# Performance work log

Hardware: AMD Instinct MI355X
Metric: run time of the kernel (lower is better)

## Reference

```python
import jax, jax.numpy as jnp
import numpy as np

ALPHA = 0.05
GDEP = 2


def conv1x1(x, w, b):
    # x: [N,C,V,L], w: [O,C], b: [O]
    return jnp.einsum('ncvl,oc->novl', x, w) + b[None, :, None, None]


def setup_inputs() -> dict:
    key = jax.random.key(0)
    ks = jax.random.split(key, 9)
    N, C, V, L = 32, 32, 400, 12
    c_out = 32
    cat = (GDEP + 1) * C
    s = 0.05
    return {
        'x': jax.random.normal(ks[0], (N, C, V, L), jnp.float32),
        'w_lin1': jax.random.normal(ks[1], (C, C), jnp.float32) * s,
        'b_lin1': jnp.zeros((C,), jnp.float32),
        'w_lin2': jax.random.normal(ks[2], (C, C), jnp.float32) * s,
        'b_lin2': jnp.zeros((C,), jnp.float32),
        'w_mlp1': jax.random.normal(ks[3], (c_out, cat), jnp.float32) * s,
        'b_mlp1': jnp.zeros((c_out,), jnp.float32),
        'w_mlp2': jax.random.normal(ks[4], (c_out, cat), jnp.float32) * s,
        'b_mlp2': jnp.zeros((c_out,), jnp.float32),
    }


def reference(x, w_lin1, b_lin1, w_lin2, b_lin2, w_mlp1, b_mlp1, w_mlp2, b_mlp2):
    # dynamic adjacency: adj[n,v,w,l] = sum_c x1[n,c,v,l] * x2[n,c,w,l]
    x1 = jnp.tanh(conv1x1(x, w_lin1, b_lin1))
    x2 = jnp.tanh(conv1x1(x, w_lin2, b_lin2))
    adj = jnp.einsum('ncvl,ncwl->nvwl', x1, x2)  # [N,V,V,L]
    adj0 = jax.nn.softmax(adj, axis=2)
    adj1 = jax.nn.softmax(jnp.swapaxes(adj, 1, 2), axis=2)

    def diffuse(a):
        h = x
        out = [h]
        for _ in range(GDEP):
            # nconv: h[n,c,w,l] = sum_v h[n,c,v,l] * a[n,v,w,l]
            h = ALPHA * x + (1.0 - ALPHA) * jnp.einsum('ncvl,nvwl->ncwl', h, a)
            out.append(h)
        return jnp.concatenate(out, axis=1)  # [N,(GDEP+1)*C,V,L]

    ho1 = conv1x1(diffuse(adj0), w_mlp1, b_mlp1)
    ho2 = conv1x1(diffuse(adj1), w_mlp2, b_mlp2)
    return ho1 + ho2
```

## Files before the change

kernel.cpp:

```cpp
#include <hip/hip_runtime.h>
#include <stdint.h>

#define TT 1024
#define AL 0.05f
#define OM 0.95f
#define STRD 408
#define LOG2E 1.4426950408889634f

typedef short s4v __attribute__((ext_vector_type(4)));
typedef short s8v __attribute__((ext_vector_type(8)));
typedef float f4v __attribute__((ext_vector_type(4)));
typedef float f16v __attribute__((ext_vector_type(16)));
typedef int   i2v __attribute__((ext_vector_type(2)));

#define MF32(a,b,c) __builtin_amdgcn_mfma_f32_32x32x16_bf16(a,b,c,0,0,0)
#define MF16(a,b,c) __builtin_amdgcn_mfma_f32_16x16x32_bf16(a,b,c,0,0,0)

#if __has_builtin(__builtin_amdgcn_exp2f)
#define E2(x) __builtin_amdgcn_exp2f(x)
#else
#define E2(x) exp2f(x)
#endif

__device__ __forceinline__ uint16_t f2bf(float f){ union{float f;uint32_t i;}t; t.f=f; return (uint16_t)((t.i + 0x7fffu + ((t.i>>16)&1u))>>16); }
__device__ __forceinline__ float bf2f(uint16_t h){ union{uint32_t i;float f;}t; t.i=((uint32_t)h)<<16; return t.f; }
__device__ __forceinline__ float bfLO(uint32_t u){ union{uint32_t i;float f;}t; t.i=u<<16; return t.f; }
__device__ __forceinline__ float bfHI(uint32_t u){ union{uint32_t i;float f;}t; t.i=u&0xffff0000u; return t.f; }
__device__ __forceinline__ uint32_t cvtpk(float lo, float hi){ uint32_t r; asm("v_cvt_pk_bf16_f32 %0, %1, %2" : "=v"(r) : "v"(lo), "v"(hi)); return r; }
__device__ __forceinline__ void pl32swap(uint32_t &x, uint32_t &y){
#if __has_builtin(__builtin_amdgcn_permlane32_swap)
  i2v rr = __builtin_amdgcn_permlane32_swap((int)x, (int)y, false, false);
  x = (uint32_t)rr.x; y = (uint32_t)rr.y;
#else
  asm("v_permlane32_swap_b32 %0, %1" : "+v"(x), "+v"(y));
#endif
}
__device__ __forceinline__ float ftanh(float x){ float t = E2(2.885390081777927f*x); return __builtin_fmaf(-2.f, __builtin_amdgcn_rcpf(1.f + t), 1.f); }
__device__ __forceinline__ s8v ld8(const uint16_t* p){ return *(const s8v*)p; }
#define ROWF(e2) (((e2)&3) + 8*((e2)>>2) + 4*h2)
#define VXA(row,off) ((((row)<<5) + (off)) ^ (((row)&7)<<3))

__device__ __align__(16) float gStage[32*12*12800];

#define X1S 0
#define X2S 12800
#define XCV 25600
#define PBA 38656
#define HCV 54656
#define GCV 67712
#define RINV 80768
#define CINV 81168

__global__ __launch_bounds__(TT) void dymix(
    const float* __restrict__ x,
    const float* __restrict__ w1, const float* __restrict__ b1,
    const float* __restrict__ w2, const float* __restrict__ b2,
    const float* __restrict__ wm1, const float* __restrict__ bm1,
    const float* __restrict__ wm2, const float* __restrict__ bm2)
{
  __shared__ __align__(16) uint16_t S[81568];

  const int blk = blockIdx.x;
  const int xcd = blk & 7, slot = blk >> 3;
  const int n = xcd*4 + slot/12;
  const int l = slot - (slot/12)*12;
  const int t = threadIdx.x;
  const int wv = t >> 6;
  const int lane = t & 63;
  const int q  = lane >> 4;
  const int r  = lane & 15;
  const int h2 = lane >> 5;
  const int m32 = lane & 31;
  const long xbase = (long)n*153600 + l;

  for (int i = t; i < 12800; i += TT) {
    int c = i / 400, v = i - c*400;
    S[XCV + c*STRD + v] = f2bf(x[xbase + (long)i*12]);
  }
  __syncthreads();

  for (int i = t; i < 12800; i += TT) { int v = i>>5, c = i&31; S[PBA + VXA(v,c)] = S[XCV + c*STRD + v]; }
  for (int i = t; i < 1024; i += TT) {
    int o = i>>5, c = i&31;
    S[PBA + 12800 + o*40 + c] = f2bf(w1[i]);
    S[PBA + 14080 + o*40 + c] = f2bf(w2[i]);
  }
  if (t < 32) { ((float*)(S+PBA+15360))[t] = b1[t]; ((float*)(S+PBA+15424))[t] = b2[t]; }
  __syncthreads();

  #pragma unroll
  for (int j = 0; j < 2; ++j) {
    int u = wv + 16*j;
    if (u < 24) {
      int nt = u >> 1, li = u & 1;
      const uint16_t* W = S + PBA + 12800 + li*1280;
      const float* bfp = (const float*)(S + PBA + 15360 + li*64);
      uint16_t* dst = S + (li ? X2S : X1S);
      const float osc = li ? 1.f : LOG2E;
      f16v z = {};
      #pragma unroll
      for (int kk = 0; kk < 2; ++kk) {
        s8v a = ld8(W + m32*40 + kk*16 + h2*8);
        s8v b = ld8(S + PBA + VXA(nt*32 + m32, kk*16 + h2*8));
        z = MF32(a, b, z);
      }
      int v = nt*32 + m32;
      #pragma unroll
      for (int g = 0; g < 4; ++g) {
        float p0 = ftanh(z[4*g+0] + bfp[8*g+4*h2+0]) * osc;
        float p1 = ftanh(z[4*g+1] + bfp[8*g+4*h2+1]) * osc;
        float p2 = ftanh(z[4*g+2] + bfp[8*g+4*h2+2]) * osc;
        float p3 = ftanh(z[4*g+3] + bfp[8*g+4*h2+3]) * osc;
        uint2 d; d.x = cvtpk(p0,p1); d.y = cvtpk(p2,p3);
        *(uint2*)(dst + VXA(v, 8*g + 4*h2)) = d;
      }
    } else if (u < 28) {
      int li = (u-24)>>1, mt = u&1;
      const uint16_t* W = S + PBA + 12800 + li*1280;
      const float* bfp = (const float*)(S + PBA + 15360 + li*64);
      uint16_t* dst = S + (li ? X2S : X1S);
      const float osc = li ? 1.f : LOG2E;
      s8v a = ld8(W + (mt*16 + r)*40 + q*8);
      s8v b = ld8(S + PBA + VXA(384 + r, q*8));
      f4v z4 = {}; z4 = MF16(a, b, z4);
      float p0 = ftanh(z4[0] + bfp[mt*16+q*4+0]) * osc;
      float p1 = ftanh(z4[1] + bfp[mt*16+q*4+1]) * osc;
      float p2 = ftanh(z4[2] + bfp[mt*16+q*4+2]) * osc;
      float p3 = ftanh(z4[3] + bfp[mt*16+q*4+3]) * osc;
      uint2 d; d.x = cvtpk(p0,p1); d.y = cvtpk(p2,p3);
      *(uint2*)(dst + VXA(384 + r, mt*16 + q*4)) = d;
    }
  }
  s8v xf0, xf1, xft;
  {
    int m0 = (wv < 12) ? wv : 0;
    xf0 = ld8(S + PBA + VXA(m0*32 + m32, h2*8));
    xf1 = ld8(S + PBA + VXA(m0*32 + m32, 16 + h2*8));
    xft = ld8(S + PBA + VXA(384 + r, q*8));
  }
  __syncthreads();

  float* rsf = (float*)(S + HCV);
  float* csf = rsf + 400;
  for (int i = t; i < 400; i += TT) csf[i] = 0.f;
  __syncthreads();
  {
    s8v av[2]; f4v rac[2] = {{},{}};
    #pragma unroll
    for (int jj = 0; jj < 2; ++jj) { int vt = wv + 16*jj; if (vt < 25) av[jj] = ld8(S + X1S + VXA(vt*16 + r, q*8)); }
    for (int wt = 0; wt < 25; ++wt) {
      s8v b = ld8(S + X2S + VXA(wt*16 + r, q*8));
      float cp = 0.f;
      #pragma unroll
      for (int jj = 0; jj < 2; ++jj) {
        int vt = wv + 16*jj;
        if (vt < 25) {
          f4v z = {}; z = MF16(av[jj], b, z);
          #pragma unroll
          for (int e = 0; e < 4; ++e) { float ev = E2(z[e]); rac[jj][e] += ev; cp += ev; }
        }
      }
      cp += __shfl_xor(cp, 16); cp += __shfl_xor(cp, 32);
      if (q == 0) atomicAdd(&csf[wt*16 + r], cp);
    }
    #pragma unroll
    for (int jj = 0; jj < 2; ++jj) {
      int vt = wv + 16*jj;
      if (vt < 25) {
        #pragma unroll
        for (int e = 0; e < 4; ++e) {
          float s = rac[jj][e];
          s += __shfl_xor(s,1); s += __shfl_xor(s,2); s += __shfl_xor(s,4); s += __shfl_xor(s,8);
          if (r == 0) rsf[vt*16 + q*4 + e] = s;
        }
      }
    }
  }
  __syncthreads();
  for (int i = t; i < 400; i += TT) { S[RINV + i] = f2bf(1.f/rsf[i]); S[CINV + i] = f2bf(1.f/csf[i]); }
  __syncthreads();

  f16v acc[2];
  for (int step = 0; step < 2; ++step) {
    { f16v zv = {}; acc[0]=zv; acc[1]=zv; }
    const uint16_t* AH = S + (step ? HCV : XCV);
    const uint16_t* AG = S + (step ? GCV : XCV);
    for (int sb = 0; sb < 13; ++sb) {
      const int vbase = sb*32;
      const bool lastsb = (sb == 12);
      const int kmax = lastsb ? 1 : 2;
      s8v fr[2][2];
      uint2 td0[2], td1[2];
      #pragma unroll
      for (int jj = 0; jj < 2; ++jj) {
        int g = wv + 16*jj;
        if (g >= 26) continue;
        int chain = (g < 13) ? 0 : 1;
        int uu = g - 13*chain;
        const uint16_t* sa = S + (chain ? X2S : X1S);
        const uint16_t* sb2 = S + (chain ? X1S : X2S);
        const int scl = chain ? CINV : RINV;
        if (uu < 12) {
          s8v a0 = ld8(sa + VXA(vbase + m32, h2*8));
          s8v a1 = ld8(sa + VXA(vbase + m32, 16 + h2*8));
          s8v b0 = ld8(sb2 + VXA(uu*32 + m32, h2*8));
          s8v b1 = ld8(sb2 + VXA(uu*32 + m32, 16 + h2*8));
          f16v z = {}; z = MF32(a0, b0, z); z = MF32(a1, b1, z);
          #pragma unroll
          for (int k = 0; k < 2; ++k) {
            if (k < kmax) {
              const uint16_t* spt = S + scl + vbase + 16*k + 4*h2;
              uint32_t sAB = *(const uint32_t*)(spt);
              uint32_t sCD = *(const uint32_t*)(spt + 2);
              uint32_t sEF = *(const uint32_t*)(spt + 8);
              uint32_t sGH = *(const uint32_t*)(spt + 10);
              uint32_t C0 = cvtpk(E2(z[8*k+0])*bfLO(sAB), E2(z[8*k+1])*bfHI(sAB));
              uint32_t C1 = cvtpk(E2(z[8*k+2])*bfLO(sCD), E2(z[8*k+3])*bfHI(sCD));
              uint32_t C2 = cvtpk(E2(z[8*k+4])*bfLO(sEF), E2(z[8*k+5])*bfHI(sEF));
              uint32_t C3 = cvtpk(E2(z[8*k+6])*bfLO(sGH), E2(z[8*k+7])*bfHI(sGH));
              pl32swap(C0, C2);
              pl32swap(C1, C3);
              union { uint32_t d[4]; s8v v8; } F;
              F.d[0] = C0; F.d[1] = C1; F.d[2] = C2; F.d[3] = C3;
              fr[jj][k] = F.v8;
            }
          }
        } else {
          s8v bT = ld8(sb2 + VXA(384 + r, q*8));
          td1[jj].x = 0u; td1[jj].y = 0u;
          {
            s8v a = ld8(sa + VXA(vbase + r, q*8));
            f4v z4 = {}; z4 = MF16(a, bT, z4);
            float p0 = E2(z4[0]) * bf2f(S[scl + vbase + q*4 + 0]);
            float p1 = E2(z4[1]) * bf2f(S[scl + vbase + q*4 + 1]);
            float p2 = E2(z4[2]) * bf2f(S[scl + vbase + q*4 + 2]);
            float p3 = E2(z4[3]) * bf2f(S[scl + vbase + q*4 + 3]);
            td0[jj].x = cvtpk(p0,p1); td0[jj].y = cvtpk(p2,p3);
          }
          if (!lastsb) {
            s8v a = ld8(sa + VXA(vbase + 16 + r, q*8));
            f4v z4 = {}; z4 = MF16(a, bT, z4);
            float p0 = E2(z4[0]) * bf2f(S[scl + vbase + 16 + q*4 + 0]);
            float p1 = E2(z4[1]) * bf2f(S[scl + vbase + 16 + q*4 + 1]);
            float p2 = E2(z4[2]) * bf2f(S[scl + vbase + 16 + q*4 + 2]);
            float p3 = E2(z4[3]) * bf2f(S[scl + vbase + 16 + q*4 + 3]);
            td1[jj].x = cvtpk(p0,p1); td1[jj].y = cvtpk(p2,p3);
          }
        }
      }
      #pragma unroll
      for (int jj = 0; jj < 2; ++jj) {
        int g = wv + 16*jj;
        if (g >= 26) continue;
        int chain = (g < 13) ? 0 : 1;
        int uu = g - 13*chain;
        const uint16_t* Acv = chain ? AG : AH;
        if (uu < 12) {
          #pragma unroll
          for (int k = 0; k < 2; ++k) {
            if (k < kmax) {
              s8v a = ld8(Acv + m32*STRD + vbase + k*16 + h2*8);
              acc[jj] = MF32(a, fr[jj][k], acc[jj]);
            }
          }
        } else {
          const int src0 = (((q<<1)) & 3)*16 + r;
          const int src1 = (((q<<1)+1) & 3)*16 + r;
          uint32_t a0x = (uint32_t)__shfl((int)td0[jj].x, src0);
          uint32_t a0y = (uint32_t)__shfl((int)td0[jj].y, src0);
          uint32_t a1x = (uint32_t)__shfl((int)td1[jj].x, src0);
          uint32_t a1y = (uint32_t)__shfl((int)td1[jj].y, src0);
          uint32_t b0x = (uint32_t)__shfl((int)td0[jj].x, src1);
          uint32_t b0y = (uint32_t)__shfl((int)td0[jj].y, src1);
          uint32_t b1x = (uint32_t)__shfl((int)td1[jj].x, src1);
          uint32_t b1y = (uint32_t)__shfl((int)td1[jj].y, src1);
          const bool hi = (q >= 2);
          union { uint32_t u[4]; s8v v8; } B;
          B.u[0] = hi ? a1x : a0x;
          B.u[1] = hi ? a1y : a0y;
          B.u[2] = hi ? b1x : b0x;
          B.u[3] = hi ? b1y : b0y;
          #pragma unroll
          for (int mt2 = 0; mt2 < 2; ++mt2) {
            int koff = (lastsb && q >= 2) ? 0 : q*8;
            s8v a = ld8(Acv + (mt2*16 + r)*STRD + vbase + koff);
            f4v c4 = { acc[jj][4*mt2+0], acc[jj][4*mt2+1], acc[jj][4*mt2+2], acc[jj][4*mt2+3] };
            c4 = MF16(a, B.v8, c4);
            acc[jj][4*mt2+0]=c4[0]; acc[jj][4*mt2+1]=c4[1]; acc[jj][4*mt2+2]=c4[2]; acc[jj][4*mt2+3]=c4[3];
          }
        }
      }
    }
    __syncthreads();
    if (step == 0) {
      #pragma unroll
      for (int jj = 0; jj < 2; ++jj) {
        int g = wv + 16*jj;
        if (g >= 26) continue;
        int chain = (g < 13) ? 0 : 1;
        int uu = g - 13*chain;
        uint16_t* dst = S + (chain ? GCV : HCV);
        if (uu < 12) {
          int w = uu*32 + m32;
          #pragma unroll
          for (int e2 = 0; e2 < 16; ++e2) {
            int c = ROWF(e2);
            dst[c*STRD + w] = f2bf(AL*bf2f(S[XCV + c*STRD + w]) + OM*acc[jj][e2]);
          }
        } else {
          int w = 384 + r;
          #pragma unroll
          for (int mt2 = 0; mt2 < 2; ++mt2)
            #pragma unroll
            for (int e = 0; e < 4; ++e) {
              int c = mt2*16 + q*4 + e;
              dst[c*STRD + w] = f2bf(AL*bf2f(S[XCV + c*STRD + w]) + OM*acc[jj][4*mt2+e]);
            }
        }
      }
      __syncthreads();
    }
  }

  for (int i = t; i < 12800; i += TT) {
    int v = i >> 5, c = i & 31;
    int d = VXA(v, c);
    S[X1S + d] = S[HCV + c*STRD + v];
    S[X2S + d] = S[GCV + c*STRD + v];
  }
  #pragma unroll
  for (int jj = 0; jj < 2; ++jj) {
    int g = wv + 16*jj;
    if (g >= 26) continue;
    int chain = (g < 13) ? 0 : 1;
    int uu = g - 13*chain;
    uint16_t* dst = S + (chain ? PBA : XCV);
    if (uu < 12) {
      int w = uu*32 + m32;
      #pragma unroll
      for (int gg = 0; gg < 4; ++gg) {
        uint2 d;
        d.x = cvtpk(OM*acc[jj][4*gg+0], OM*acc[jj][4*gg+1]);
        d.y = cvtpk(OM*acc[jj][4*gg+2], OM*acc[jj][4*gg+3]);
        *(uint2*)(dst + VXA(w, 8*gg + 4*h2)) = d;
      }
    } else {
      int w = 384 + r;
      #pragma unroll
      for (int mt2 = 0; mt2 < 2; ++mt2) {
        uint2 d;
        d.x = cvtpk(OM*acc[jj][4*mt2+0], OM*acc[jj][4*mt2+1]);
        d.y = cvtpk(OM*acc[jj][4*mt2+2], OM*acc[jj][4*mt2+3]);
        *(uint2*)(dst + VXA(w, mt2*16 + q*4)) = d;
      }
    }
  }
  __syncthreads();
  for (int i = t; i < 1024; i += TT) {
    int o = i >> 5, c = i & 31;
    float h2w = wm1[o*96 + 64 + c], g2w = wm2[o*96 + 64 + c];
    S[HCV +        o*40 + c] = f2bf(wm1[o*96 + c] + wm2[o*96 + c] + AL*(h2w + g2w));
    S[HCV + 1280 + o*40 + c] = f2bf(wm1[o*96 + 32 + c]);
    S[HCV + 2560 + o*40 + c] = f2bf(h2w);
    S[HCV + 3840 + o*40 + c] = f2bf(wm2[o*96 + 32 + c]);
    S[HCV + 5120 + o*40 + c] = f2bf(g2w);
  }
  if (t < 32) ((float*)(S + HCV + 6400))[t] = bm1[t] + bm2[t];
  __syncthreads();

  {
    const float* boF = (const float*)(S + HCV + 6400);
    float* oSl = gStage + (long)(n*12 + l)*12800;
    const int fb[5] = { 0, X1S, XCV, X2S, PBA };
    int m = wv;
    if (m < 12) {
      f16v z = {};
      #pragma unroll
      for (int p = 0; p < 5; ++p) {
        #pragma unroll
        for (int kk = 0; kk < 2; ++kk) {
          s8v a = ld8(S + HCV + p*1280 + m32*40 + kk*16 + h2*8);
          s8v b;
          if (p == 0) b = kk ? xf1 : xf0;
          else        b = ld8(S + fb[p] + VXA(m*32 + m32, kk*16 + h2*8));
          z = MF32(a, b, z);
        }
      }
      int v = m*32 + m32;
      #pragma unroll
      for (int e2 = 0; e2 < 16; ++e2) {
        int o = ROWF(e2);
        oSl[o*400 + v] = z[e2] + boF[o];
      }
    } else if (m < 14) {
      int mt = m - 12;
      f4v z4 = {};
      #pragma unroll
      for (int p = 0; p < 5; ++p) {
        s8v a = ld8(S + HCV + p*1280 + (mt*16 + r)*40 + q*8);
        s8v b = (p == 0) ? xft : ld8(S + fb[p] + VXA(384 + r, q*8));
        z4 = MF16(a, b, z4);
      }
      #pragma unroll
      for (int e = 0; e < 4; ++e) {
        int o = mt*16 + q*4 + e;
        oSl[o*400 + 384 + r] = z4[e] + boF[o];
      }
    }
  }
}

__global__ __launch_bounds__(256) void finT(float* __restrict__ out) {
  int idx = blockIdx.x*256 + threadIdx.x;
  int n = idx / 12800, ov = idx - n*12800;
  const float* src = gStage + (long)n*153600 + ov;
  float vals[12];
  #pragma unroll
  for (int l = 0; l < 12; ++l) vals[l] = src[(long)l*12800];
  float4* dst = (float4*)(out + (long)idx*12);
  dst[0] = make_float4(vals[0],vals[1],vals[2],vals[3]);
  dst[1] = make_float4(vals[4],vals[5],vals[6],vals[7]);
  dst[2] = make_float4(vals[8],vals[9],vals[10],vals[11]);
}

extern "C" void kernel_launch(void* const* d_in, const int* in_sizes, int n_in,
                              void* d_out, int out_size, void* d_ws, size_t ws_size,
                              hipStream_t stream) {
  (void)in_sizes; (void)n_in; (void)out_size; (void)d_ws; (void)ws_size;
  dymix<<<dim3(384), dim3(TT), 0, stream>>>(
      (const float*)d_in[0],
      (const float*)d_in[1], (const float*)d_in[2],
      (const float*)d_in[3], (const float*)d_in[4],
      (const float*)d_in[5], (const float*)d_in[6],
      (const float*)d_in[7], (const float*)d_in[8]);
  finT<<<dim3(1600), dim3(256), 0, stream>>>((float*)d_out);
}
```

Baseline: 231.5 us.

## Use FP8 MFMA for adjacency scores and shrink LDS footprint

Stores the tanh projections x1/x2 as FP8 in shared memory and computes the adjacency logits with FP8 MFMA instead of BF16. It also restructures the shared-memory layout to roughly half the size. Weights are now read directly from global memory instead of staged copies. The final MLP is split into two passes that reuse buffers, with the second pass accumulating into the global staging output. The aim is to raise occupancy and cut LDS traffic and MFMA cost, at the risk of reduced accuracy in the softmax logits and an extra global read-modify-write.

```diff
diff --git a/kernel.cpp b/kernel.cpp
--- a/kernel.cpp
+++ b/kernel.cpp
@@ -15,6 +15,8 @@
 
 #define MF32(a,b,c) __builtin_amdgcn_mfma_f32_32x32x16_bf16(a,b,c,0,0,0)
 #define MF16(a,b,c) __builtin_amdgcn_mfma_f32_16x16x32_bf16(a,b,c,0,0,0)
+#define MFP32(a,b,c) __builtin_amdgcn_mfma_f32_32x32x16_fp8_fp8(a,b,c,0,0,0)
+#define MFP16(a,b,c) __builtin_amdgcn_mfma_f32_16x16x32_fp8_fp8(a,b,c,0,0,0)
 
 #if __has_builtin(__builtin_amdgcn_exp2f)
 #define E2(x) __builtin_amdgcn_exp2f(x)
@@ -37,19 +39,50 @@
 }
 __device__ __forceinline__ float ftanh(float x){ float t = E2(2.885390081777927f*x); return __builtin_fmaf(-2.f, __builtin_amdgcn_rcpf(1.f + t), 1.f); }
 __device__ __forceinline__ s8v ld8(const uint16_t* p){ return *(const s8v*)p; }
+
+__device__ __forceinline__ uint32_t sw1fp8(float f){
+  union{float f;uint32_t u;}t; t.f=f;
+  uint32_t sgn=(t.u>>24)&0x80u; uint32_t a=t.u&0x7fffffffu;
+  union{uint32_t u;float f;}af; af.u=a;
+  if(af.f>448.f) return sgn|0x7eu;
+  if(af.f<0.001953125f){ int q=(int)(af.f*512.f+0.5f); if(q>7)q=7; return sgn|(uint32_t)q; }
+  uint32_t lsb=(a>>20)&1u; a+=0x0007ffffu+lsb;
+  int ex=(int)(a>>23)-120; uint32_t man=(a>>20)&7u;
+  if(ex>15||(ex==15&&man==7u)) return sgn|0x7eu;
+  if(ex<=0){ int q=(int)(af.f*512.f+0.5f); if(q>7)q=7; return sgn|(uint32_t)q; }
+  return sgn|((uint32_t)ex<<3)|man;
+}
+__device__ __forceinline__ uint32_t pk4fp8(float a,float b,float c,float d){
+#if __has_builtin(__builtin_amdgcn_cvt_pk_fp8_f32)
+  int v = __builtin_amdgcn_cvt_pk_fp8_f32(a,b,0,false);
+  v = __builtin_amdgcn_cvt_pk_fp8_f32(c,d,v,true);
+  return (uint32_t)v;
+#else
+  return sw1fp8(a) | (sw1fp8(b)<<8) | (sw1fp8(c)<<16) | (sw1fp8(d)<<24);
+#endif
+}
+__device__ __forceinline__ s8v packw8(float4 f0, float4 f1){
+  union{uint32_t d[4]; s8v v8;} A;
+  A.d[0]=cvtpk(f0.x,f0.y); A.d[1]=cvtpk(f0.z,f0.w);
+  A.d[2]=cvtpk(f1.x,f1.y); A.d[3]=cvtpk(f1.z,f1.w);
+  return A.v8;
+}
+
 #define ROWF(e2) (((e2)&3) + 8*((e2)>>2) + 4*h2)
 #define VXA(row,off) ((((row)<<5) + (off)) ^ (((row)&7)<<3))
+#define VX8(row,b) ((((row)<<5) + (b)) ^ (((row)&3)<<4))
 
 __device__ __align__(16) float gStage[32*12*12800];
 
-#define X1S 0
-#define X2S 12800
-#define XCV 25600
-#define PBA 38656
-#define HCV 54656
-#define GCV 67712
-#define RINV 80768
-#define CINV 81168
+#define X1B 0
+#define X2B 12800
+#define XCV 12800
+#define GCV 25856
+#define XTU 25856
+#define RINV 38912
+#define CINV 39312
+#define HV 0
+#define F2V 12800
 
 __global__ __launch_bounds__(TT) void dymix(
     const float* __restrict__ x,
@@ -58,7 +91,8 @@
     const float* __restrict__ wm1, const float* __restrict__ bm1,
     const float* __restrict__ wm2, const float* __restrict__ bm2)
 {
-  __shared__ __align__(16) uint16_t S[81568];
+  __shared__ __align__(16) uint16_t S[39712];
+  uint8_t* S8 = (uint8_t*)S;
 
   const int blk = blockIdx.x;
   const int xcd = blk & 7, slot = blk >> 3;
@@ -79,13 +113,7 @@
   }
   __syncthreads();
 
-  for (int i = t; i < 12800; i += TT) { int v = i>>5, c = i&31; S[PBA + VXA(v,c)] = S[XCV + c*STRD + v]; }
-  for (int i = t; i < 1024; i += TT) {
-    int o = i>>5, c = i&31;
-    S[PBA + 12800 + o*40 + c] = f2bf(w1[i]);
-    S[PBA + 14080 + o*40 + c] = f2bf(w2[i]);
-  }
-  if (t < 32) { ((float*)(S+PBA+15360))[t] = b1[t]; ((float*)(S+PBA+15424))[t] = b2[t]; }
+  for (int i = t; i < 12800; i += TT) { int v = i>>5, c = i&31; S[XTU + VXA(v,c)] = S[XCV + c*STRD + v]; }
   __syncthreads();
 
   #pragma unroll
@@ -93,69 +121,71 @@
     int u = wv + 16*j;
     if (u < 24) {
       int nt = u >> 1, li = u & 1;
-      const uint16_t* W = S + PBA + 12800 + li*1280;
-      const float* bfp = (const float*)(S + PBA + 15360 + li*64);
-      uint16_t* dst = S + (li ? X2S : X1S);
+      const float* wsrc = li ? w2 : w1;
+      const float* bsrc = li ? b2 : b1;
+      uint8_t* dst8 = S8 + (li ? X2B : X1B);
       const float osc = li ? 1.f : LOG2E;
       f16v z = {};
       #pragma unroll
       for (int kk = 0; kk < 2; ++kk) {
-        s8v a = ld8(W + m32*40 + kk*16 + h2*8);
-        s8v b = ld8(S + PBA + VXA(nt*32 + m32, kk*16 + h2*8));
+        const float* wp = wsrc + m32*32 + kk*16 + h2*8;
+        s8v a = packw8(*(const float4*)(wp), *(const float4*)(wp+4));
+        s8v b = ld8(S + XTU + VXA(nt*32 + m32, kk*16 + h2*8));
         z = MF32(a, b, z);
       }
       int v = nt*32 + m32;
       #pragma unroll
       for (int g = 0; g < 4; ++g) {
-        float p0 = ftanh(z[4*g+0] + bfp[8*g+4*h2+0]) * osc;
-        float p1 = ftanh(z[4*g+1] + bfp[8*g+4*h2+1]) * osc;
-        float p2 = ftanh(z[4*g+2] + bfp[8*g+4*h2+2]) * osc;
-        float p3 = ftanh(z[4*g+3] + bfp[8*g+4*h2+3]) * osc;
-        uint2 d; d.x = cvtpk(p0,p1); d.y = cvtpk(p2,p3);
-        *(uint2*)(dst + VXA(v, 8*g + 4*h2)) = d;
+        float4 bv = *(const float4*)(bsrc + 8*g + 4*h2);
+        float p0 = ftanh(z[4*g+0] + bv.x) * osc;
+        float p1 = ftanh(z[4*g+1] + bv.y) * osc;
+        float p2 = ftanh(z[4*g+2] + bv.z) * osc;
+        float p3 = ftanh(z[4*g+3] + bv.w) * osc;
+        *(uint32_t*)(dst8 + VX8(v, 8*g + 4*h2)) = pk4fp8(p0,p1,p2,p3);
       }
     } else if (u < 28) {
       int li = (u-24)>>1, mt = u&1;
-      const uint16_t* W = S + PBA + 12800 + li*1280;
-      const float* bfp = (const float*)(S + PBA + 15360 + li*64);
-      uint16_t* dst = S + (li ? X2S : X1S);
+      const float* wsrc = li ? w2 : w1;
+      const float* bsrc = li ? b2 : b1;
+      uint8_t* dst8 = S8 + (li ? X2B : X1B);
       const float osc = li ? 1.f : LOG2E;
-      s8v a = ld8(W + (mt*16 + r)*40 + q*8);
-      s8v b = ld8(S + PBA + VXA(384 + r, q*8));
+      const float* wp = wsrc + (mt*16 + r)*32 + q*8;
+      s8v a = packw8(*(const float4*)(wp), *(const float4*)(wp+4));
+      s8v b = ld8(S + XTU + VXA(384 + r, q*8));
       f4v z4 = {}; z4 = MF16(a, b, z4);
-      float p0 = ftanh(z4[0] + bfp[mt*16+q*4+0]) * osc;
-      float p1 = ftanh(z4[1] + bfp[mt*16+q*4+1]) * osc;
-      float p2 = ftanh(z4[2] + bfp[mt*16+q*4+2]) * osc;
-      float p3 = ftanh(z4[3] + bfp[mt*16+q*4+3]) * osc;
-      uint2 d; d.x = cvtpk(p0,p1); d.y = cvtpk(p2,p3);
-      *(uint2*)(dst + VXA(384 + r, mt*16 + q*4)) = d;
+      float4 bv = *(const float4*)(bsrc + mt*16 + q*4);
+      float p0 = ftanh(z4[0] + bv.x) * osc;
+      float p1 = ftanh(z4[1] + bv.y) * osc;
+      float p2 = ftanh(z4[2] + bv.z) * osc;
+      float p3 = ftanh(z4[3] + bv.w) * osc;
+      *(uint32_t*)(dst8 + VX8(384 + r, mt*16 + q*4)) = pk4fp8(p0,p1,p2,p3);
     }
   }
   s8v xf0, xf1, xft;
   {
     int m0 = (wv < 12) ? wv : 0;
-    xf0 = ld8(S + PBA + VXA(m0*32 + m32, h2*8));
-    xf1 = ld8(S + PBA + VXA(m0*32 + m32, 16 + h2*8));
-    xft = ld8(S + PBA + VXA(384 + r, q*8));
-  }
-  __syncthreads();
-
-  float* rsf = (float*)(S + HCV);
+    xf0 = ld8(S + XTU + VXA(m0*32 + m32, h2*8));
+    xf1 = ld8(S + XTU + VXA(m0*32 + m32, 16 + h2*8));
+    xft = ld8(S + XTU + VXA(384 + r, q*8));
+  }
+  __syncthreads();
+
+  float* rsf = (float*)(S + GCV);
   float* csf = rsf + 400;
   for (int i = t; i < 400; i += TT) csf[i] = 0.f;
   __syncthreads();
   {
-    s8v av[2]; f4v rac[2] = {{},{}};
+    long av8[2]; f4v rac[2] = {{},{}};
     #pragma unroll
-    for (int jj = 0; jj < 2; ++jj) { int vt = wv + 16*jj; if (vt < 25) av[jj] = ld8(S + X1S + VXA(vt*16 + r, q*8)); }
+    for (int jj = 0; jj < 2; ++jj) { int vt = wv + 16*jj; if (vt < 25) av8[jj] = *(const long*)(S8 + X1B + VX8(vt*16 + r, q*8)); }
     for (int wt = 0; wt < 25; ++wt) {
-      s8v b = ld8(S + X2S + VXA(wt*16 + r, q*8));
+      long b8 = *(const long*)(S8 + X2B + VX8(wt*16 + r, q*8));
       float cp = 0.f;
       #pragma unroll
       for (int jj = 0; jj < 2; ++jj) {
         int vt = wv + 16*jj;
         if (vt < 25) {
-          f4v z = {}; z = MF16(av[jj], b, z);
+          f4v z = {}; z = MFP16(av8[jj], b8, z);
           #pragma unroll
           for (int e = 0; e < 4; ++e) { float ev = E2(z[e]); rac[jj][e] += ev; cp += ev; }
         }
@@ -183,7 +213,7 @@
   f16v acc[2];
   for (int step = 0; step < 2; ++step) {
     { f16v zv = {}; acc[0]=zv; acc[1]=zv; }
-    const uint16_t* AH = S + (step ? HCV : XCV);
+    const uint16_t* AH = S + XCV;
     const uint16_t* AG = S + (step ? GCV : XCV);
     for (int sb = 0; sb < 13; ++sb) {
       const int vbase = sb*32;
@@ -197,15 +227,15 @@
         if (g >= 26) continue;
         int chain = (g < 13) ? 0 : 1;
         int uu = g - 13*chain;
-        const uint16_t* sa = S + (chain ? X2S : X1S);
-        const uint16_t* sb2 = S + (chain ? X1S : X2S);
+        const uint8_t* sa8 = S8 + (chain ? X2B : X1B);
+        const uint8_t* sb8 = S8 + (chain ? X1B : X2B);
         const int scl = chain ? CINV : RINV;
         if (uu < 12) {
-          s8v a0 = ld8(sa + VXA(vbase + m32, h2*8));
-          s8v a1 = ld8(sa + VXA(vbase + m32, 16 + h2*8));
-          s8v b0 = ld8(sb2 + VXA(uu*32 + m32, h2*8));
-          s8v b1 = ld8(sb2 + VXA(uu*32 + m32, 16 + h2*8));
-          f16v z = {}; z = MF32(a0, b0, z); z = MF32(a1, b1, z);
+          long a0 = *(const long*)(sa8 + VX8(vbase + m32, h2*8));
+          long a1 = *(const long*)(sa8 + VX8(vbase + m32, 16 + h2*8));
+          long b0 = *(const long*)(sb8 + VX8(uu*32 + m32, h2*8));
+          long b1 = *(const long*)(sb8 + VX8(uu*32 + m32, 16 + h2*8));
+          f16v z = {}; z = MFP32(a0, b0, z); z = MFP32(a1, b1, z);
           #pragma unroll
           for (int k = 0; k < 2; ++k) {
             if (k < kmax) {
@@ -226,11 +256,11 @@
             }
           }
         } else {
-          s8v bT = ld8(sb2 + VXA(384 + r, q*8));
+          long bT = *(const long*)(sb8 + VX8(384 + r, q*8));
           td1[jj].x = 0u; td1[jj].y = 0u;
           {
-            s8v a = ld8(sa + VXA(vbase + r, q*8));
-            f4v z4 = {}; z4 = MF16(a, bT, z4);
+            long a = *(const long*)(sa8 + VX8(vbase + r, q*8));
+            f4v z4 = {}; z4 = MFP16(a, bT, z4);
             float p0 = E2(z4[0]) * bf2f(S[scl + vbase + q*4 + 0]);
             float p1 = E2(z4[1]) * bf2f(S[scl + vbase + q*4 + 1]);
             float p2 = E2(z4[2]) * bf2f(S[scl + vbase + q*4 + 2]);
@@ -238,8 +268,8 @@
             td0[jj].x = cvtpk(p0,p1); td0[jj].y = cvtpk(p2,p3);
           }
           if (!lastsb) {
-            s8v a = ld8(sa + VXA(vbase + 16 + r, q*8));
-            f4v z4 = {}; z4 = MF16(a, bT, z4);
+            long a = *(const long*)(sa8 + VX8(vbase + 16 + r, q*8));
+            f4v z4 = {}; z4 = MFP16(a, bT, z4);
             float p0 = E2(z4[0]) * bf2f(S[scl + vbase + 16 + q*4 + 0]);
             float p1 = E2(z4[1]) * bf2f(S[scl + vbase + 16 + q*4 + 1]);
             float p2 = E2(z4[2]) * bf2f(S[scl + vbase + 16 + q*4 + 2]);
@@ -299,13 +329,12 @@
         if (g >= 26) continue;
         int chain = (g < 13) ? 0 : 1;
         int uu = g - 13*chain;
-        uint16_t* dst = S + (chain ? GCV : HCV);
         if (uu < 12) {
           int w = uu*32 + m32;
           #pragma unroll
           for (int e2 = 0; e2 < 16; ++e2) {
             int c = ROWF(e2);
-            dst[c*STRD + w] = f2bf(AL*bf2f(S[XCV + c*STRD + w]) + OM*acc[jj][e2]);
+            acc[jj][e2] = AL*bf2f(S[XCV + c*STRD + w]) + OM*acc[jj][e2];
           }
         } else {
           int w = 384 + r;
@@ -314,27 +343,42 @@
             #pragma unroll
             for (int e = 0; e < 4; ++e) {
               int c = mt2*16 + q*4 + e;
-              dst[c*STRD + w] = f2bf(AL*bf2f(S[XCV + c*STRD + w]) + OM*acc[jj][4*mt2+e]);
+              acc[jj][4*mt2+e] = AL*bf2f(S[XCV + c*STRD + w]) + OM*acc[jj][4*mt2+e];
             }
         }
       }
       __syncthreads();
-    }
-  }
-
-  for (int i = t; i < 12800; i += TT) {
-    int v = i >> 5, c = i & 31;
-    int d = VXA(v, c);
-    S[X1S + d] = S[HCV + c*STRD + v];
-    S[X2S + d] = S[GCV + c*STRD + v];
-  }
+      #pragma unroll
+      for (int jj = 0; jj < 2; ++jj) {
+        int g = wv + 16*jj;
+        if (g >= 26) continue;
+        int chain = (g < 13) ? 0 : 1;
+        int uu = g - 13*chain;
+        uint16_t* dst = S + (chain ? GCV : XCV);
+        if (uu < 12) {
+          int w = uu*32 + m32;
+          #pragma unroll
+          for (int e2 = 0; e2 < 16; ++e2) { int c = ROWF(e2); dst[c*STRD + w] = f2bf(acc[jj][e2]); }
+        } else {
+          int w = 384 + r;
+          #pragma unroll
+          for (int mt2 = 0; mt2 < 2; ++mt2)
+            #pragma unroll
+            for (int e = 0; e < 4; ++e) { int c = mt2*16 + q*4 + e; dst[c*STRD + w] = f2bf(acc[jj][4*mt2+e]); }
+        }
+      }
+      __syncthreads();
+    }
+  }
+
+  for (int i = t; i < 12800; i += TT) { int v = i >> 5, c = i & 31; S[HV + VXA(v,c)] = S[XCV + c*STRD + v]; }
+  __syncthreads();
   #pragma unroll
   for (int jj = 0; jj < 2; ++jj) {
     int g = wv + 16*jj;
-    if (g >= 26) continue;
-    int chain = (g < 13) ? 0 : 1;
-    int uu = g - 13*chain;
-    uint16_t* dst = S + (chain ? PBA : XCV);
+    if (g >= 13) continue;
+    int uu = g;
+    uint16_t* dst = S + F2V;
     if (uu < 12) {
       int w = uu*32 + m32;
       #pragma unroll
@@ -356,56 +400,127 @@
     }
   }
   __syncthreads();
-  for (int i = t; i < 1024; i += TT) {
-    int o = i >> 5, c = i & 31;
-    float h2w = wm1[o*96 + 64 + c], g2w = wm2[o*96 + 64 + c];
-    S[HCV +        o*40 + c] = f2bf(wm1[o*96 + c] + wm2[o*96 + c] + AL*(h2w + g2w));
-    S[HCV + 1280 + o*40 + c] = f2bf(wm1[o*96 + 32 + c]);
-    S[HCV + 2560 + o*40 + c] = f2bf(h2w);
-    S[HCV + 3840 + o*40 + c] = f2bf(wm2[o*96 + 32 + c]);
-    S[HCV + 5120 + o*40 + c] = f2bf(g2w);
-  }
-  if (t < 32) ((float*)(S + HCV + 6400))[t] = bm1[t] + bm2[t];
-  __syncthreads();
-
+
+  float* oSl = gStage + (long)(n*12 + l)*12800;
   {
-    const float* boF = (const float*)(S + HCV + 6400);
-    float* oSl = gStage + (long)(n*12 + l)*12800;
-    const int fb[5] = { 0, X1S, XCV, X2S, PBA };
     int m = wv;
     if (m < 12) {
       f16v z = {};
       #pragma unroll
-      for (int p = 0; p < 5; ++p) {
+      for (int p = 0; p < 3; ++p) {
         #pragma unroll
         for (int kk = 0; kk < 2; ++kk) {
-          s8v a = ld8(S + HCV + p*1280 + m32*40 + kk*16 + h2*8);
-          s8v b;
-          if (p == 0) b = kk ? xf1 : xf0;
-          else        b = ld8(S + fb[p] + VXA(m*32 + m32, kk*16 + h2*8));
+          const float* wp = wm1 + m32*96 + p*32 + kk*16 + h2*8;
+          float4 f0 = *(const float4*)(wp), f1 = *(const float4*)(wp+4);
+          if (p == 0) {
+            const float* wp2 = wm1 + m32*96 + 64 + kk*16 + h2*8;
+            float4 g0 = *(const float4*)(wp2), g1 = *(const float4*)(wp2+4);
+            f0.x += AL*g0.x; f0.y += AL*g0.y; f0.z += AL*g0.z; f0.w += AL*g0.w;
+            f1.x += AL*g1.x; f1.y += AL*g1.y; f1.z += AL*g1.z; f1.w += AL*g1.w;
+          }
+          s8v a = packw8(f0, f1);
+          s8v b = (p == 0) ? (kk ? xf1 : xf0)
+                           : ld8(S + (p == 1 ? HV : F2V) + VXA(m*32 + m32, kk*16 + h2*8));
           z = MF32(a, b, z);
         }
       }
       int v = m*32 + m32;
       #pragma unroll
-      for (int e2 = 0; e2 < 16; ++e2) {
-        int o = ROWF(e2);
-        oSl[o*400 + v] = z[e2] + boF[o];
-      }
+      for (int e2 = 0; e2 < 16; ++e2) { int o = ROWF(e2); oSl[o*400 + v] = z[e2] + bm1[o] + bm2[o]; }
     } else if (m < 14) {
       int mt = m - 12;
       f4v z4 = {};
       #pragma unroll
-      for (int p = 0; p < 5; ++p) {
-        s8v a = ld8(S + HCV + p*1280 + (mt*16 + r)*40 + q*8);
-        s8v b = (p == 0) ? xft : ld8(S + fb[p] + VXA(384 + r, q*8));
+      for (int p = 0; p < 3; ++p) {
+        const float* wp = wm1 + (mt*16 + r)*96 + p*32 + q*8;
+        float4 f0 = *(const float4*)(wp), f1 = *(const float4*)(wp+4);
+        if (p == 0) {
+          const float* wp2 = wm1 + (mt*16 + r)*96 + 64 + q*8;
+          float4 g0 = *(const float4*)(wp2), g1 = *(const float4*)(wp2+4);
+          f0.x += AL*g0.x; f0.y += AL*g0.y; f0.z += AL*g0.z; f0.w += AL*g0.w;
+          f1.x += AL*g1.x; f1.y += AL*g1.y; f1.z += AL*g1.z; f1.w += AL*g1.w;
+        }
+        s8v a = packw8(f0, f1);
+        s8v b = (p == 0) ? xft : ld8(S + (p == 1 ? HV : F2V) + VXA(384 + r, q*8));
         z4 = MF16(a, b, z4);
       }
       #pragma unroll
-      for (int e = 0; e < 4; ++e) {
-        int o = mt*16 + q*4 + e;
-        oSl[o*400 + 384 + r] = z4[e] + boF[o];
-      }
+      for (int e = 0; e < 4; ++e) { int o = mt*16 + q*4 + e; oSl[o*400 + 384 + r] = z4[e] + bm1[o] + bm2[o]; }
+    }
+  }
+  __syncthreads();
+  for (int i = t; i < 12800; i += TT) { int v = i >> 5, c = i & 31; S[HV + VXA(v,c)] = S[GCV + c*STRD + v]; }
+  #pragma unroll
+  for (int jj = 0; jj < 2; ++jj) {
+    int g = wv + 16*jj;
+    if (g < 13 || g >= 26) continue;
+    int uu = g - 13;
+    uint16_t* dst = S + F2V;
+    if (uu < 12) {
+      int w = uu*32 + m32;
+      #pragma unroll
+      for (int gg = 0; gg < 4; ++gg) {
+        uint2 d;
+        d.x = cvtpk(OM*acc[jj][4*gg+0], OM*acc[jj][4*gg+1]);
+        d.y = cvtpk(OM*acc[jj][4*gg+2], OM*acc[jj][4*gg+3]);
+        *(uint2*)(dst + VXA(w, 8*gg + 4*h2)) = d;
+      }
+    } else {
+      int w = 384 + r;
+      #pragma unroll
+      for (int mt2 = 0; mt2 < 2; ++mt2) {
+        uint2 d;
+        d.x = cvtpk(OM*acc[jj][4*mt2+0], OM*acc[jj][4*mt2+1]);
+        d.y = cvtpk(OM*acc[jj][4*mt2+2], OM*acc[jj][4*mt2+3]);
+        *(uint2*)(dst + VXA(w, mt2*16 + q*4)) = d;
+      }
+    }
+  }
+  __syncthreads();
+  {
+    int m = wv;
+    if (m < 12) {
+      f16v z = {};
+      #pragma unroll
+      for (int p = 0; p < 3; ++p) {
+        #pragma unroll
+        for (int kk = 0; kk < 2; ++kk) {
+          const float* wp = wm2 + m32*96 + p*32 + kk*16 + h2*8;
+          float4 f0 = *(const float4*)(wp), f1 = *(const float4*)(wp+4);
+          if (p == 0) {
+            const float* wp2 = wm2 + m32*96 + 64 + kk*16 + h2*8;
+            float4 g0 = *(const float4*)(wp2), g1 = *(const float4*)(wp2+4);
+            f0.x += AL*g0.x; f0.y += AL*g0.y; f0.z += AL*g0.z; f0.w += AL*g0.w;
+            f1.x += AL*g1.x; f1.y += AL*g1.y; f1.z += AL*g1.z; f1.w += AL*g1.w;
+          }
+          s8v a = packw8(f0, f1);
+          s8v b = (p == 0) ? (kk ? xf1 : xf0)
+                           : ld8(S + (p == 1 ? HV : F2V) + VXA(m*32 + m32, kk*16 + h2*8));
+          z = MF32(a, b, z);
+        }
+      }
+      int v = m*32 + m32;
+      #pragma unroll
+      for (int e2 = 0; e2 < 16; ++e2) { int o = ROWF(e2); oSl[o*400 + v] += z[e2]; }
+    } else if (m < 14) {
+      int mt = m - 12;
+      f4v z4 = {};
+      #pragma unroll
+      for (int p = 0; p < 3; ++p) {
+        const float* wp = wm2 + (mt*16 + r)*96 + p*32 + q*8;
+        float4 f0 = *(const float4*)(wp), f1 = *(const float4*)(wp+4);
+        if (p == 0) {
+          const float* wp2 = wm2 + (mt*16 + r)*96 + 64 + q*8;
+          float4 g0 = *(const float4*)(wp2), g1 = *(const float4*)(wp2+4);
+          f0.x += AL*g0.x; f0.y += AL*g0.y; f0.z += AL*g0.z; f0.w += AL*g0.w;
+          f1.x += AL*g1.x; f1.y += AL*g1.y; f1.z += AL*g1.z; f1.w += AL*g1.w;
+        }
+        s8v a = packw8(f0, f1);
+        s8v b = (p == 0) ? xft : ld8(S + (p == 1 ? HV : F2V) + VXA(384 + r, q*8));
+        z4 = MF16(a, b, z4);
+      }
+      #pragma unroll
+      for (int e = 0; e < 4; ++e) { int o = mt*16 + q*4 + e; oSl[o*400 + 384 + r] += z4[e]; }
     }
   }
 }
```

Result: slower. 254.2 us (+9.8%).
